# Kernel optimization log

Measured on AMD Instinct MI355X. Metric: run time of the kernel, lower is better.

Reference implementation:

```python
import jax, jax.numpy as jnp
import numpy as np

D_MODEL = 512
N_HEADS = 8
HEAD_DIM = D_MODEL // N_HEADS
NEG_INF = -1e9


def setup_inputs() -> dict:
    key = jax.random.key(0)
    ks = jax.random.split(key, 12)
    B, N, M = 8, 2048, 2048
    inp = {
        'query': jax.random.normal(ks[0], (B, D_MODEL, N), jnp.float32),
        'key': jax.random.normal(ks[1], (B, D_MODEL, M), jnp.float32),
        'value': jax.random.normal(ks[2], (B, D_MODEL, M), jnp.float32),
        'query_mask': jnp.ones((B, N), jnp.float32),
        'key_value_mask': jnp.ones((B, M), jnp.float32),
        # Conv1d(d_model, d_model, kernel_size=1) == pointwise linear: W [out, in], b [out]
        'Wq': jax.random.normal(ks[3], (D_MODEL, D_MODEL), jnp.float32) / np.sqrt(D_MODEL),
        'bq': jax.random.normal(ks[4], (D_MODEL,), jnp.float32) * 0.01,
        'Wk': jax.random.normal(ks[5], (D_MODEL, D_MODEL), jnp.float32) / np.sqrt(D_MODEL),
        'bk': jax.random.normal(ks[6], (D_MODEL,), jnp.float32) * 0.01,
        'Wv': jax.random.normal(ks[7], (D_MODEL, D_MODEL), jnp.float32) / np.sqrt(D_MODEL),
        'bv': jax.random.normal(ks[8], (D_MODEL,), jnp.float32) * 0.01,
        'Wm': jax.random.normal(ks[9], (D_MODEL, D_MODEL), jnp.float32) / np.sqrt(D_MODEL),
        'bm': jax.random.normal(ks[10], (D_MODEL,), jnp.float32) * 0.01,
    }
    return inp


def _pointwise(W, b, x):
    # Conv1d k=1 over [B, C_in, N] -> [B, C_out, N]
    return jnp.einsum('oi,bin->bon', W, x) + b[None, :, None]


def reference(query, key, value, query_mask, key_value_mask,
              Wq, bq, Wk, bk, Wv, bv, Wm, bm):
    B = query.shape[0]
    N = query.shape[2]
    M = key.shape[2]
    # project and split heads: [B, head_dim, n_heads, seq]
    q = _pointwise(Wq, bq, query).reshape(B, HEAD_DIM, N_HEADS, N)
    k = _pointwise(Wk, bk, key).reshape(B, HEAD_DIM, N_HEADS, M)
    v = _pointwise(Wv, bv, value).reshape(B, HEAD_DIM, N_HEADS, M)
    # scores [B, H, N, M], scaled by sqrt(head_dim) (query.shape[1] post-split)
    scores = jnp.einsum('bdhn,bdhm->bhnm', q, k) / jnp.sqrt(jnp.float32(HEAD_DIM))
    # dual mask: outer product of key_value_mask [B,1,1,M] and query_mask [B,1,N,1]
    mask = key_value_mask[:, None, None, :] * query_mask[:, None, :, None]
    scores = jnp.where(mask > 0, scores, NEG_INF)
    prob = jax.nn.softmax(scores, axis=-1)  # [B, H, N, M]
    x = jnp.einsum('bhnm,bdhm->bdhn', prob, v)  # [B, head_dim, H, N]
    out = _pointwise(Wm, bm, x.reshape(B, D_MODEL, N))
    return out
```

## Files before the change

kernel.cpp:

```cpp
#include <hip/hip_runtime.h>


typedef _Float16 f16;
typedef _Float16 f16x4 __attribute__((ext_vector_type(4)));
typedef _Float16 f16x8 __attribute__((ext_vector_type(8)));
typedef float f32x4 __attribute__((ext_vector_type(4)));

#define D_MODEL 512
#define HD 64
#define SEQ 2048
#define QSCL 0.18033688011112042f
#define KVNEG -1.4426950409e9f
#define FMAXB -6.0f

__global__ __launch_bounds__(256) void k_transpose(
    const float* __restrict__ q, const float* __restrict__ k, const float* __restrict__ v,
    f16* __restrict__ XT)
{
  __shared__ __align__(16) f16 Ts[64][72];
  int t = threadIdx.x;
  int nt = blockIdx.x, ct = blockIdx.y, z = blockIdx.z;
  int src = z >> 3, b = z & 7;
  const float* S = (src == 0) ? q : (src == 1) ? k : v;
  {
    int cr = t >> 2, ns = t & 3;
    const float* p = S + ((size_t)b * D_MODEL + ct * 64 + cr) * SEQ + nt * 64 + ns * 16;
    f32x4 a0 = *(const f32x4*)(p);
    f32x4 a1 = *(const f32x4*)(p + 4);
    f32x4 a2 = *(const f32x4*)(p + 8);
    f32x4 a3 = *(const f32x4*)(p + 12);
    f16x8 h0, h1;
#pragma unroll
    for (int j = 0; j < 4; ++j) { h0[j] = (f16)a0[j]; h0[4 + j] = (f16)a1[j]; h1[j] = (f16)a2[j]; h1[4 + j] = (f16)a3[j]; }
    *(f16x8*)&Ts[cr][ns * 16] = h0;
    *(f16x8*)&Ts[cr][ns * 16 + 8] = h1;
  }
  __syncthreads();
  {
    int nr = t >> 2, cs = t & 3;
    f16x8 h0, h1;
#pragma unroll
    for (int j = 0; j < 8; ++j) h0[j] = Ts[cs * 16 + j][nr];
#pragma unroll
    for (int j = 0; j < 8; ++j) h1[j] = Ts[cs * 16 + 8 + j][nr];
    f16* dst = XT + (((size_t)z) * SEQ + nt * 64 + nr) * D_MODEL + ct * 64 + cs * 16;
    *(f16x8*)dst = h0;
    *(f16x8*)(dst + 8) = h1;
  }
}

__global__ __launch_bounds__(256) void k_wconv(
    const float* __restrict__ Wq, const float* __restrict__ Wk, const float* __restrict__ Wv,
    const float* __restrict__ Wm, f16* __restrict__ W3, f16* __restrict__ Wmh)
{
  int idx = blockIdx.x * 256 + threadIdx.x;
  if (idx < 262144) {
    W3[idx] = (f16)Wq[idx];
    W3[262144 + idx] = (f16)Wk[idx];
    W3[524288 + idx] = (f16)Wv[idx];
    int o = idx >> 9, c = idx & 511;
    int h = c & 7, d = c >> 3;
    Wmh[((size_t)h * 512 + o) * 64 + d] = (f16)Wm[idx];
  }
}

__global__ __launch_bounds__(256, 2) void k_proj(
    const f16* __restrict__ W3, const float* __restrict__ bq, const float* __restrict__ bk,
    const float* __restrict__ bv, const f16* __restrict__ XT,
    f16* __restrict__ Qt, f16* __restrict__ Kt, f16* __restrict__ Vh)
{
  __shared__ __align__(16) char smem[36864];
  f16 (*As)[72] = (f16(*)[72])smem;
  f16 (*Bs)[72] = (f16(*)[72])(smem + 18432);
  f16 (*Ls)[136] = (f16(*)[136])smem;

  int t = threadIdx.x;
  int proj = blockIdx.z, b = blockIdx.y;
  int ot = blockIdx.x & 3, ntile = blockIdx.x >> 2;
  int w = t >> 6, ln = t & 63, i16 = ln & 15, q4 = ln >> 4;
  int ow = w >> 1, nw = w & 1;

  const f16* Wp = W3 + (size_t)proj * 262144;
  const f16* Xp = XT + ((size_t)proj * 8 + b) * (size_t)SEQ * D_MODEL;

  f32x4 acc[4][4];
#pragma unroll
  for (int x = 0; x < 4; ++x)
#pragma unroll
    for (int y = 0; y < 4; ++y) acc[x][y] = (f32x4){0.f, 0.f, 0.f, 0.f};

  int srow = t >> 1, shalf = t & 1;
  for (int kc = 0; kc < 8; ++kc) {
    __syncthreads();
    const f16* Ap = Wp + ((size_t)(ot * 128 + srow)) * 512 + kc * 64 + shalf * 32;
#pragma unroll
    for (int s8 = 0; s8 < 4; ++s8)
      *(f32x4*)&As[srow][shalf * 32 + s8 * 8] = *(const f32x4*)(Ap + s8 * 8);
    const f16* Bp = Xp + ((size_t)(ntile * 128 + srow)) * 512 + kc * 64 + shalf * 32;
#pragma unroll
    for (int s8 = 0; s8 < 4; ++s8)
      *(f32x4*)&Bs[srow][shalf * 32 + s8 * 8] = *(const f32x4*)(Bp + s8 * 8);
    __syncthreads();
#pragma unroll
    for (int kk = 0; kk < 2; ++kk) {
      f16x8 af[4], bf[4];
#pragma unroll
      for (int x = 0; x < 4; ++x) af[x] = *(const f16x8*)&As[ow * 64 + x * 16 + i16][kk * 32 + q4 * 8];
#pragma unroll
      for (int y = 0; y < 4; ++y) bf[y] = *(const f16x8*)&Bs[nw * 64 + y * 16 + i16][kk * 32 + q4 * 8];
#pragma unroll
      for (int x = 0; x < 4; ++x)
#pragma unroll
        for (int y = 0; y < 4; ++y)
          acc[x][y] = __builtin_amdgcn_mfma_f32_16x16x32_f16(af[x], bf[y], acc[x][y], 0, 0, 0);
    }
  }

  const float* bias = (proj == 0) ? bq : (proj == 1) ? bk : bv;
  float scl = (proj == 0) ? QSCL : 1.0f;
  __syncthreads();
#pragma unroll
  for (int x = 0; x < 4; ++x) {
    f32x4 bb = *(const f32x4*)(bias + ot * 128 + ow * 64 + x * 16 + q4 * 4);
#pragma unroll
    for (int y = 0; y < 4; ++y)
#pragma unroll
      for (int r = 0; r < 4; ++r)
        Ls[ow * 64 + x * 16 + q4 * 4 + r][nw * 64 + y * 16 + i16] = (f16)((acc[x][y][r] + bb[r]) * scl);
  }
  __syncthreads();
  if (proj < 2) {
    f16* dst = (proj == 0) ? Qt : Kt;
    int n = t >> 1, seg = t & 1;
#pragma unroll
    for (int h = 0; h < 8; ++h) {
      f16x8 g;
#pragma unroll
      for (int j = 0; j < 8; ++j) g[j] = Ls[8 * (seg * 8 + j) + h][n];
      f16* dp = dst + (((size_t)((b * 8 + h) * 4 + ot)) * 2048 + ntile * 128 + n) * 16 + seg * 8;
      *(f16x8*)dp = g;
    }
  } else {
#pragma unroll
    for (int p = 0; p < 8; ++p) {
      int ol = (t >> 4) + 16 * p;
      int ch = t & 15;
      int og = ot * 128 + ol;
      int h = og & 7, d = og >> 3;
      f16* dp = Vh + (((size_t)(b * 8 + h)) * HD + d) * SEQ + ntile * 128 + ch * 8;
      *(f32x4*)dp = *(const f32x4*)&Ls[ol][ch * 8];
    }
  }
}

__global__ __launch_bounds__(256, 4) void k_attn(
    const f16* __restrict__ Qt, const f16* __restrict__ Kt, const f16* __restrict__ Vh,
    const float* __restrict__ qmask, const float* __restrict__ kvmask,
    f16* __restrict__ O)
{
  __shared__ __align__(16) char smem[18432];
  f16 (*Qs)[72] = (f16(*)[72])smem;
  f16 (*Ks)[72] = (f16(*)[72])smem;
  f16 (*Vs)[72] = (f16(*)[72])(smem + 9216);

  int t = threadIdx.x;
  int bh = blockIdx.x >> 4;
  int b = bh >> 3;
  int n0 = (blockIdx.x & 15) * 128;
  int w = t >> 6, ln = t & 63, i16 = ln & 15, q4 = ln >> 4;

  const f16* Qb = Qt + (size_t)bh * 131072;
  const f16* Kb = Kt + (size_t)bh * 131072;
  const f16* Vb = Vh + (size_t)bh * HD * SEQ;
  const float* kvp = kvmask + (size_t)b * SEQ;

#pragma unroll
  for (int p = 0; p < 4; ++p) {
    int tid = p * 256 + t;
    int n = tid & 127, cx = tid >> 7;
    *(f32x4*)&Qs[n][cx * 8] =
        *(const f32x4*)(Qb + ((size_t)((cx >> 1) * 2048 + n0 + n)) * 16 + (cx & 1) * 8);
  }
  __syncthreads();
  f16x8 qf[2][2];
#pragma unroll
  for (int nt = 0; nt < 2; ++nt)
#pragma unroll
    for (int kc = 0; kc < 2; ++kc)
      qf[nt][kc] = *(const f16x8*)&Qs[w * 32 + nt * 16 + i16][kc * 32 + q4 * 8];
#pragma unroll
  for (int nt = 0; nt < 2; ++nt) {
    float qok = qmask[(size_t)b * SEQ + n0 + w * 32 + nt * 16 + i16];
    f16 qz = (qok > 0.f) ? (f16)1 : (f16)0;
    qf[nt][0] *= qz;
    qf[nt][1] *= qz;
  }

  f32x4 acc_o[4][2];
#pragma unroll
  for (int dt = 0; dt < 4; ++dt)
#pragma unroll
    for (int nt = 0; nt < 2; ++nt) acc_o[dt][nt] = (f32x4){0.f, 0.f, 0.f, 0.f};
  float rsum2[2] = {0.f, 0.f};

  for (int it = 0; it < 32; ++it) {
    int m0 = it * 64;
    __syncthreads();
#pragma unroll
    for (int p = 0; p < 2; ++p) {
      int tid = p * 256 + t;
      int cx = tid >> 6, nk = tid & 63;
      *(f32x4*)&Ks[nk][cx * 8] =
          *(const f32x4*)(Kb + ((size_t)((cx >> 1) * 2048 + m0 + nk)) * 16 + (cx & 1) * 8);
      int vrow = tid >> 3, vch = tid & 7;
      *(f32x4*)&Vs[vrow][vch * 8] = *(const f32x4*)(Vb + (size_t)vrow * SEQ + m0 + vch * 8);
    }
    __syncthreads();

    f32x4 bias[4];
#pragma unroll
    for (int mt = 0; mt < 4; ++mt) {
      f32x4 kv = *(const f32x4*)(kvp + m0 + mt * 16 + q4 * 4);
#pragma unroll
      for (int r = 0; r < 4; ++r) bias[mt][r] = (kv[r] > 0.f) ? FMAXB : KVNEG;
    }

    f32x4 s[2][4];
#pragma unroll
    for (int mt = 0; mt < 4; ++mt) {
      f16x8 kf0 = *(const f16x8*)&Ks[mt * 16 + i16][q4 * 8];
      f16x8 kf1 = *(const f16x8*)&Ks[mt * 16 + i16][32 + q4 * 8];
      f32x4 a0 = __builtin_amdgcn_mfma_f32_16x16x32_f16(kf0, qf[0][0], bias[mt], 0, 0, 0);
      s[0][mt] = __builtin_amdgcn_mfma_f32_16x16x32_f16(kf1, qf[0][1], a0, 0, 0, 0);
      f32x4 a1 = __builtin_amdgcn_mfma_f32_16x16x32_f16(kf0, qf[1][0], bias[mt], 0, 0, 0);
      s[1][mt] = __builtin_amdgcn_mfma_f32_16x16x32_f16(kf1, qf[1][1], a1, 0, 0, 0);
    }

    f16x4 pf[4][2];
#pragma unroll
    for (int nt = 0; nt < 2; ++nt) {
      float rs = 0.f;
#pragma unroll
      for (int mt = 0; mt < 4; ++mt) {
        float p0 = __builtin_amdgcn_exp2f(s[nt][mt][0]);
        float p1 = __builtin_amdgcn_exp2f(s[nt][mt][1]);
        float p2 = __builtin_amdgcn_exp2f(s[nt][mt][2]);
        float p3 = __builtin_amdgcn_exp2f(s[nt][mt][3]);
        rs += (p0 + p1) + (p2 + p3);
        f16x4 pv;
        pv[0] = (f16)p0; pv[1] = (f16)p1; pv[2] = (f16)p2; pv[3] = (f16)p3;
        pf[mt][nt] = pv;
      }
      rsum2[nt] += rs;
    }

#pragma unroll
    for (int dt = 0; dt < 4; ++dt) {
      f16x4 vf[4];
#pragma unroll
      for (int mt = 0; mt < 4; ++mt)
        vf[mt] = *(const f16x4*)&Vs[dt * 16 + i16][mt * 16 + q4 * 4];
#pragma unroll
      for (int nt = 0; nt < 2; ++nt) {
        f32x4 o = acc_o[dt][nt];
#pragma unroll
        for (int mt = 0; mt < 4; ++mt)
          o = __builtin_amdgcn_mfma_f32_16x16x16f16(vf[mt], pf[mt][nt], o, 0, 0, 0);
        acc_o[dt][nt] = o;
      }
    }
  }

  __syncthreads();
  f16 (*Os)[72] = (f16(*)[72])(smem + w * 4608);
#pragma unroll
  for (int nt = 0; nt < 2; ++nt) {
    float l = rsum2[nt];
    l += __shfl_xor(l, 16, 64);
    l += __shfl_xor(l, 32, 64);
    float inv = 1.f / l;
#pragma unroll
    for (int dt = 0; dt < 4; ++dt) {
      f16x4 o4;
#pragma unroll
      for (int r = 0; r < 4; ++r) o4[r] = (f16)(acc_o[dt][nt][r] * inv);
      *(f16x4*)&Os[nt * 16 + i16][dt * 16 + q4 * 4] = o4;
    }
  }
  __syncthreads();
  f16* Ob = O + ((size_t)bh * SEQ + n0 + w * 32) * HD;
#pragma unroll
  for (int p = 0; p < 4; ++p) {
    int row = (ln >> 3) + 8 * p, ch = ln & 7;
    *(f32x4*)(Ob + (size_t)row * HD + ch * 8) = *(const f32x4*)&Os[row][ch * 8];
  }
}

__global__ __launch_bounds__(256, 2) void k_out(
    const f16* __restrict__ Wmh, const float* __restrict__ bm,
    const f16* __restrict__ O, float* __restrict__ out)
{
  __shared__ __align__(16) char smem[20480];
  f16 (*As)[40] = (f16(*)[40])smem;
  f16 (*Bs)[40] = (f16(*)[40])(smem + 10240);

  int t = threadIdx.x;
  int b = blockIdx.y;
  int ot = blockIdx.x & 3, ntile = blockIdx.x >> 2;
  int w = t >> 6, ln = t & 63, i16 = ln & 15, q4 = ln >> 4;
  int ow = w >> 1, nw = w & 1;

  f32x4 acc[4][4];
#pragma unroll
  for (int x = 0; x < 4; ++x)
#pragma unroll
    for (int y = 0; y < 4; ++y) acc[x][y] = (f32x4){0.f, 0.f, 0.f, 0.f};

  int srow = t >> 1, sseg = t & 1;
  for (int ck = 0; ck < 16; ++ck) {
    int h = ck >> 1, dc = ck & 1;
    __syncthreads();
    const f16* Ap = Wmh + ((size_t)h * 512 + ot * 128 + srow) * 64 + dc * 32 + sseg * 16;
    *(f32x4*)&As[srow][sseg * 16] = *(const f32x4*)(Ap);
    *(f32x4*)&As[srow][sseg * 16 + 8] = *(const f32x4*)(Ap + 8);
    const f16* Bp = O + (((size_t)(b * 8 + h)) * SEQ + ntile * 128 + srow) * 64 + dc * 32 + sseg * 16;
    *(f32x4*)&Bs[srow][sseg * 16] = *(const f32x4*)(Bp);
    *(f32x4*)&Bs[srow][sseg * 16 + 8] = *(const f32x4*)(Bp + 8);
    __syncthreads();
    f16x8 af[4], bf[4];
#pragma unroll
    for (int x = 0; x < 4; ++x) af[x] = *(const f16x8*)&As[ow * 64 + x * 16 + i16][q4 * 8];
#pragma unroll
    for (int y = 0; y < 4; ++y) bf[y] = *(const f16x8*)&Bs[nw * 64 + y * 16 + i16][q4 * 8];
#pragma unroll
    for (int x = 0; x < 4; ++x)
#pragma unroll
      for (int y = 0; y < 4; ++y)
        acc[x][y] = __builtin_amdgcn_mfma_f32_16x16x32_f16(af[x], bf[y], acc[x][y], 0, 0, 0);
  }

#pragma unroll
  for (int x = 0; x < 4; ++x) {
    f32x4 bb = *(const f32x4*)(bm + ot * 128 + ow * 64 + x * 16 + q4 * 4);
#pragma unroll
    for (int y = 0; y < 4; ++y)
#pragma unroll
      for (int r = 0; r < 4; ++r) {
        int o_g = ot * 128 + ow * 64 + x * 16 + q4 * 4 + r;
        int n_g = ntile * 128 + nw * 64 + y * 16 + i16;
        out[((size_t)b * 512 + o_g) * SEQ + n_g] = acc[x][y][r] + bb[r];
      }
  }
}

extern "C" void kernel_launch(void* const* d_in, const int* in_sizes, int n_in,
                              void* d_out, int out_size, void* d_ws, size_t ws_size,
                              hipStream_t stream)
{
  const float* query  = (const float*)d_in[0];
  const float* key    = (const float*)d_in[1];
  const float* value  = (const float*)d_in[2];
  const float* qmask  = (const float*)d_in[3];
  const float* kvmask = (const float*)d_in[4];
  const float* Wq = (const float*)d_in[5];
  const float* bq = (const float*)d_in[6];
  const float* Wk = (const float*)d_in[7];
  const float* bk = (const float*)d_in[8];
  const float* Wv = (const float*)d_in[9];
  const float* bv = (const float*)d_in[10];
  const float* Wm = (const float*)d_in[11];
  const float* bm = (const float*)d_in[12];
  float* out = (float*)d_out;

  char* ws = (char*)d_ws;
  f16* XT  = (f16*)(ws);
  f16* Qt  = (f16*)(ws + 50331648);
  f16* Kt  = (f16*)(ws + 67108864);
  f16* Vh  = (f16*)(ws + 83886080);
  f16* Oat = (f16*)(ws);
  f16* W3  = (f16*)(ws + 100663296);
  f16* Wmh = (f16*)(ws + 102236160);

  k_transpose<<<dim3(32, 8, 24), 256, 0, stream>>>(query, key, value, XT);
  k_wconv<<<1024, 256, 0, stream>>>(Wq, Wk, Wv, Wm, W3, Wmh);
  k_proj<<<dim3(64, 8, 3), 256, 0, stream>>>(W3, bq, bk, bv, XT, Qt, Kt, Vh);
  k_attn<<<1024, 256, 0, stream>>>(Qt, Kt, Vh, qmask, kvmask, Oat);
  k_out<<<dim3(64, 8), 256, 0, stream>>>(Wmh, bm, Oat, out);
}
```

Measured before the change: 330.6 us.

## Register-prefetch next tiles in proj, attn, and out kernels; remap block order

Adds register-staged prefetch of the next K-chunk (proj, out) and next K/V/mask tile (attn), issuing the global loads before the MFMA loop so their latency overlaps compute. The out-projection GEMM now uses 64-wide k-chunks (8 iterations instead of 16) with a larger shared tile. Block index mapping is swapped so neighbouring blocks share weights or heads, which is meant to improve L2 reuse. k_proj's launch bound moves to 3 blocks per CU. The cost is more live registers, which risks spills or lower occupancy, and one wasted wrap-around prefetch per loop.

```diff
diff --git a/kernel.cpp b/kernel.cpp
--- a/kernel.cpp
+++ b/kernel.cpp
@@ -64,7 +64,7 @@
   }
 }
 
-__global__ __launch_bounds__(256, 2) void k_proj(
+__global__ __launch_bounds__(256, 3) void k_proj(
     const f16* __restrict__ W3, const float* __restrict__ bq, const float* __restrict__ bk,
     const float* __restrict__ bv, const f16* __restrict__ XT,
     f16* __restrict__ Qt, f16* __restrict__ Kt, f16* __restrict__ Vh)
@@ -76,7 +76,7 @@
 
   int t = threadIdx.x;
   int proj = blockIdx.z, b = blockIdx.y;
-  int ot = blockIdx.x & 3, ntile = blockIdx.x >> 2;
+  int ntile = blockIdx.x & 15, ot = blockIdx.x >> 4;
   int w = t >> 6, ln = t & 63, i16 = ln & 15, q4 = ln >> 4;
   int ow = w >> 1, nw = w & 1;
 
@@ -90,16 +90,26 @@
     for (int y = 0; y < 4; ++y) acc[x][y] = (f32x4){0.f, 0.f, 0.f, 0.f};
 
   int srow = t >> 1, shalf = t & 1;
+  const f16* Ap = Wp + ((size_t)(ot * 128 + srow)) * 512 + shalf * 32;
+  const f16* Bp = Xp + ((size_t)(ntile * 128 + srow)) * 512 + shalf * 32;
+
+  f32x4 pa[4], pb[4];
+#pragma unroll
+  for (int s8 = 0; s8 < 4; ++s8) { pa[s8] = *(const f32x4*)(Ap + s8 * 8); pb[s8] = *(const f32x4*)(Bp + s8 * 8); }
+
   for (int kc = 0; kc < 8; ++kc) {
     __syncthreads();
-    const f16* Ap = Wp + ((size_t)(ot * 128 + srow)) * 512 + kc * 64 + shalf * 32;
-#pragma unroll
-    for (int s8 = 0; s8 < 4; ++s8)
-      *(f32x4*)&As[srow][shalf * 32 + s8 * 8] = *(const f32x4*)(Ap + s8 * 8);
-    const f16* Bp = Xp + ((size_t)(ntile * 128 + srow)) * 512 + kc * 64 + shalf * 32;
-#pragma unroll
-    for (int s8 = 0; s8 < 4; ++s8)
-      *(f32x4*)&Bs[srow][shalf * 32 + s8 * 8] = *(const f32x4*)(Bp + s8 * 8);
+#pragma unroll
+    for (int s8 = 0; s8 < 4; ++s8) {
+      *(f32x4*)&As[srow][shalf * 32 + s8 * 8] = pa[s8];
+      *(f32x4*)&Bs[srow][shalf * 32 + s8 * 8] = pb[s8];
+    }
+    int kn = ((kc + 1) & 7) * 64;
+#pragma unroll
+    for (int s8 = 0; s8 < 4; ++s8) {
+      pa[s8] = *(const f32x4*)(Ap + kn + s8 * 8);
+      pb[s8] = *(const f32x4*)(Bp + kn + s8 * 8);
+    }
     __syncthreads();
 #pragma unroll
     for (int kk = 0; kk < 2; ++kk) {
@@ -164,9 +174,9 @@
   f16 (*Vs)[72] = (f16(*)[72])(smem + 9216);
 
   int t = threadIdx.x;
-  int bh = blockIdx.x >> 4;
+  int bh = blockIdx.x & 63;
   int b = bh >> 3;
-  int n0 = (blockIdx.x & 15) * 128;
+  int n0 = (blockIdx.x >> 6) * 128;
   int w = t >> 6, ln = t & 63, i16 = ln & 15, q4 = ln >> 4;
 
   const f16* Qb = Qt + (size_t)bh * 131072;
@@ -203,26 +213,51 @@
     for (int nt = 0; nt < 2; ++nt) acc_o[dt][nt] = (f32x4){0.f, 0.f, 0.f, 0.f};
   float rsum2[2] = {0.f, 0.f};
 
+  int cxA = t >> 6, nkA = t & 63;
+  int cxB = cxA + 4, nkB = nkA;
+  const f16* kAp = Kb + ((size_t)((cxA >> 1) * 2048 + nkA)) * 16 + (cxA & 1) * 8;
+  const f16* kBp = Kb + ((size_t)((cxB >> 1) * 2048 + nkB)) * 16 + (cxB & 1) * 8;
+  int vrA = t >> 3, vcA = t & 7;
+  int vrB = vrA + 32, vcB = vcA;
+  const f16* vAp = Vb + (size_t)vrA * SEQ + vcA * 8;
+  const f16* vBp = Vb + (size_t)vrB * SEQ + vcB * 8;
+
+  f32x4 ka = *(const f32x4*)(kAp);
+  f32x4 kb_ = *(const f32x4*)(kBp);
+  f32x4 va = *(const f32x4*)(vAp);
+  f32x4 vb_ = *(const f32x4*)(vBp);
+  f32x4 kv0 = *(const f32x4*)(kvp + q4 * 4);
+  f32x4 kv1 = *(const f32x4*)(kvp + 16 + q4 * 4);
+  f32x4 kv2 = *(const f32x4*)(kvp + 32 + q4 * 4);
+  f32x4 kv3 = *(const f32x4*)(kvp + 48 + q4 * 4);
+
   for (int it = 0; it < 32; ++it) {
-    int m0 = it * 64;
-    __syncthreads();
-#pragma unroll
-    for (int p = 0; p < 2; ++p) {
-      int tid = p * 256 + t;
-      int cx = tid >> 6, nk = tid & 63;
-      *(f32x4*)&Ks[nk][cx * 8] =
-          *(const f32x4*)(Kb + ((size_t)((cx >> 1) * 2048 + m0 + nk)) * 16 + (cx & 1) * 8);
-      int vrow = tid >> 3, vch = tid & 7;
-      *(f32x4*)&Vs[vrow][vch * 8] = *(const f32x4*)(Vb + (size_t)vrow * SEQ + m0 + vch * 8);
+    __syncthreads();
+    *(f32x4*)&Ks[nkA][cxA * 8] = ka;
+    *(f32x4*)&Ks[nkB][cxB * 8] = kb_;
+    *(f32x4*)&Vs[vrA][vcA * 8] = va;
+    *(f32x4*)&Vs[vrB][vcB * 8] = vb_;
+    f32x4 kc0 = kv0, kc1 = kv1, kc2 = kv2, kc3 = kv3;
+    {
+      int mn = ((it + 1) & 31) * 64;
+      ka  = *(const f32x4*)(kAp + (size_t)mn * 16);
+      kb_ = *(const f32x4*)(kBp + (size_t)mn * 16);
+      va  = *(const f32x4*)(vAp + mn);
+      vb_ = *(const f32x4*)(vBp + mn);
+      kv0 = *(const f32x4*)(kvp + mn + q4 * 4);
+      kv1 = *(const f32x4*)(kvp + mn + 16 + q4 * 4);
+      kv2 = *(const f32x4*)(kvp + mn + 32 + q4 * 4);
+      kv3 = *(const f32x4*)(kvp + mn + 48 + q4 * 4);
     }
     __syncthreads();
 
     f32x4 bias[4];
 #pragma unroll
-    for (int mt = 0; mt < 4; ++mt) {
-      f32x4 kv = *(const f32x4*)(kvp + m0 + mt * 16 + q4 * 4);
-#pragma unroll
-      for (int r = 0; r < 4; ++r) bias[mt][r] = (kv[r] > 0.f) ? FMAXB : KVNEG;
+    for (int r = 0; r < 4; ++r) {
+      bias[0][r] = (kc0[r] > 0.f) ? FMAXB : KVNEG;
+      bias[1][r] = (kc1[r] > 0.f) ? FMAXB : KVNEG;
+      bias[2][r] = (kc2[r] > 0.f) ? FMAXB : KVNEG;
+      bias[3][r] = (kc3[r] > 0.f) ? FMAXB : KVNEG;
     }
 
     f32x4 s[2][4];
@@ -300,13 +335,13 @@
     const f16* __restrict__ Wmh, const float* __restrict__ bm,
     const f16* __restrict__ O, float* __restrict__ out)
 {
-  __shared__ __align__(16) char smem[20480];
-  f16 (*As)[40] = (f16(*)[40])smem;
-  f16 (*Bs)[40] = (f16(*)[40])(smem + 10240);
+  __shared__ __align__(16) char smem[36864];
+  f16 (*As)[72] = (f16(*)[72])smem;
+  f16 (*Bs)[72] = (f16(*)[72])(smem + 18432);
 
   int t = threadIdx.x;
   int b = blockIdx.y;
-  int ot = blockIdx.x & 3, ntile = blockIdx.x >> 2;
+  int ntile = blockIdx.x & 15, ot = blockIdx.x >> 4;
   int w = t >> 6, ln = t & 63, i16 = ln & 15, q4 = ln >> 4;
   int ow = w >> 1, nw = w & 1;
 
@@ -316,27 +351,43 @@
 #pragma unroll
     for (int y = 0; y < 4; ++y) acc[x][y] = (f32x4){0.f, 0.f, 0.f, 0.f};
 
-  int srow = t >> 1, sseg = t & 1;
-  for (int ck = 0; ck < 16; ++ck) {
-    int h = ck >> 1, dc = ck & 1;
-    __syncthreads();
-    const f16* Ap = Wmh + ((size_t)h * 512 + ot * 128 + srow) * 64 + dc * 32 + sseg * 16;
-    *(f32x4*)&As[srow][sseg * 16] = *(const f32x4*)(Ap);
-    *(f32x4*)&As[srow][sseg * 16 + 8] = *(const f32x4*)(Ap + 8);
-    const f16* Bp = O + (((size_t)(b * 8 + h)) * SEQ + ntile * 128 + srow) * 64 + dc * 32 + sseg * 16;
-    *(f32x4*)&Bs[srow][sseg * 16] = *(const f32x4*)(Bp);
-    *(f32x4*)&Bs[srow][sseg * 16 + 8] = *(const f32x4*)(Bp + 8);
-    __syncthreads();
-    f16x8 af[4], bf[4];
-#pragma unroll
-    for (int x = 0; x < 4; ++x) af[x] = *(const f16x8*)&As[ow * 64 + x * 16 + i16][q4 * 8];
-#pragma unroll
-    for (int y = 0; y < 4; ++y) bf[y] = *(const f16x8*)&Bs[nw * 64 + y * 16 + i16][q4 * 8];
-#pragma unroll
-    for (int x = 0; x < 4; ++x)
-#pragma unroll
-      for (int y = 0; y < 4; ++y)
-        acc[x][y] = __builtin_amdgcn_mfma_f32_16x16x32_f16(af[x], bf[y], acc[x][y], 0, 0, 0);
+  int srow = t >> 1, shalf = t & 1;
+  const f16* Ap = Wmh + ((size_t)(ot * 128 + srow)) * 64 + shalf * 32;
+  const f16* Bp = O + (((size_t)(b * 8)) * SEQ + ntile * 128 + srow) * 64 + shalf * 32;
+
+  f32x4 pa[4], pb[4];
+#pragma unroll
+  for (int s8 = 0; s8 < 4; ++s8) { pa[s8] = *(const f32x4*)(Ap + s8 * 8); pb[s8] = *(const f32x4*)(Bp + s8 * 8); }
+
+  for (int ck = 0; ck < 8; ++ck) {
+    __syncthreads();
+#pragma unroll
+    for (int s8 = 0; s8 < 4; ++s8) {
+      *(f32x4*)&As[srow][shalf * 32 + s8 * 8] = pa[s8];
+      *(f32x4*)&Bs[srow][shalf * 32 + s8 * 8] = pb[s8];
+    }
+    {
+      size_t hn = (size_t)((ck + 1) & 7);
+#pragma unroll
+      for (int s8 = 0; s8 < 4; ++s8) {
+        pa[s8] = *(const f32x4*)(Ap + hn * 32768 + s8 * 8);
+        pb[s8] = *(const f32x4*)(Bp + hn * 131072 + s8 * 8);
+      }
+    }
+    __syncthreads();
+#pragma unroll
+    for (int kk = 0; kk < 2; ++kk) {
+      f16x8 af[4], bf[4];
+#pragma unroll
+      for (int x = 0; x < 4; ++x) af[x] = *(const f16x8*)&As[ow * 64 + x * 16 + i16][kk * 32 + q4 * 8];
+#pragma unroll
+      for (int y = 0; y < 4; ++y) bf[y] = *(const f16x8*)&Bs[nw * 64 + y * 16 + i16][kk * 32 + q4 * 8];
+#pragma unroll
+      for (int x = 0; x < 4; ++x)
+#pragma unroll
+        for (int y = 0; y < 4; ++y)
+          acc[x][y] = __builtin_amdgcn_mfma_f32_16x16x32_f16(af[x], bf[y], acc[x][y], 0, 0, 0);
+    }
   }
 
 #pragma unroll
```

Measured after the change: 445.3 us. 34.7% more time.
